# Kernel optimization log

Measured on AMD Instinct MI355X. Metric: run time of the kernel, lower is better.

Reference implementation:

```python
import jax, jax.numpy as jnp
from jax import lax
import numpy as np

DG = 2          # deformable groups
KH = KW = 3     # kernel size
KK = KH * KW
PAD = 1


def setup_inputs() -> dict:
    key = jax.random.key(0)
    k1, k2, k3 = jax.random.split(key, 3)
    B, C, H, W = 4, 64, 128, 128
    O = 64
    x = jax.random.normal(k1, (B, C, H, W), jnp.float32)
    # original inits offset weights to 0 (degenerate: plain conv); use small random
    # weights instead so the irregular bilinear-gather path is actually exercised.
    w_off = jax.random.normal(k2, (DG * 2 * KK, C, KH, KW), jnp.float32) * 0.05
    w_def = jax.random.normal(k3, (O, C, KH, KW), jnp.float32) * (1.0 / np.sqrt(C * KK))
    return {"x": x, "w_off": w_off, "w_def": w_def}


def _deform_conv(x, w_off, w_def):
    B, C, H, W = x.shape
    O = w_def.shape[0]
    Cg = C // DG

    # offset = offset_conv(x): stride 1, pad 1, no bias -> [B, DG*2*KK, H, W]
    offset = lax.conv_general_dilated(
        x, w_off, window_strides=(1, 1), padding=((PAD, PAD), (PAD, PAD)),
        dimension_numbers=("NCHW", "OIHW", "NCHW"))
    # DCN layout: per group, per kernel tap k, channel 2k = dy, 2k+1 = dx
    off = offset.reshape(B, DG, KK, 2, H, W)

    ki, kj = jnp.meshgrid(jnp.arange(KH), jnp.arange(KW), indexing="ij")
    ki = (ki.reshape(KK) - PAD).astype(x.dtype)   # kernel row offsets -1..1
    kj = (kj.reshape(KK) - PAD).astype(x.dtype)
    hh = jnp.arange(H, dtype=x.dtype)
    ww = jnp.arange(W, dtype=x.dtype)

    # sampling positions [B, DG, KK, H, W]
    py = off[:, :, :, 0] + ki[None, None, :, None, None] + hh[None, None, None, :, None]
    px = off[:, :, :, 1] + kj[None, None, :, None, None] + ww[None, None, None, None, :]

    y0 = jnp.floor(py).astype(jnp.int32)
    x0 = jnp.floor(px).astype(jnp.int32)
    dy = py - y0.astype(x.dtype)
    dx = px - x0.astype(x.dtype)

    x_g = x.reshape(B, DG, Cg, H * W)

    def gather(yi, xi):
        # zero padding outside the image
        valid = ((yi >= 0) & (yi < H) & (xi >= 0) & (xi < W)).astype(x.dtype)
        yc = jnp.clip(yi, 0, H - 1)
        xc = jnp.clip(xi, 0, W - 1)
        idx = (yc * W + xc).reshape(B, DG, 1, KK * H * W)
        v = jnp.take_along_axis(x_g, idx, axis=3).reshape(B, DG, Cg, KK, H, W)
        return v * valid[:, :, None]  # broadcast over channel axis

    # bilinear interpolation at learned offset positions
    val = (gather(y0, x0) * ((1 - dy) * (1 - dx))[:, :, None]
           + gather(y0, x0 + 1) * ((1 - dy) * dx)[:, :, None]
           + gather(y0 + 1, x0) * (dy * (1 - dx))[:, :, None]
           + gather(y0 + 1, x0 + 1) * (dy * dx)[:, :, None])

    # weighted accumulation: conv groups = 1, channel dim = DG*Cg
    w = w_def.reshape(O, DG, Cg, KK)
    return jnp.einsum("bgckhw,ogck->bohw", val, w)


def reference(x, w_off, w_def):
    return _deform_conv(x, w_off, w_def)
```

## Files before the change

### kernel.cpp

```cpp
#include <hip/hip_runtime.h>
#include <hip/hip_bf16.h>

typedef _Float16 f16x8 __attribute__((ext_vector_type(8)));
typedef _Float16 f16x2 __attribute__((ext_vector_type(2)));
typedef float f32x4  __attribute__((ext_vector_type(4)));

#define Bn 4
#define Cn 64
#define Hn 128
#define Wn 128
#define HWn 16384

#define XT_BYTES    (Bn*HWn*Cn*2)
#define PKDEF_BYTES (18*4*64*8*2)

static __device__ __forceinline__ unsigned pk_f16(float lo, float hi) {
  union { _Float16 h[2]; unsigned u; } cv;
  cv.h[0] = (_Float16)lo; cv.h[1] = (_Float16)hi;
  return cv.u;
}

__global__ __launch_bounds__(256) void transpose_cast(const float* __restrict__ x,
                                                      ushort* __restrict__ xt) {
  __shared__ float tile[64][65];
  const int t = threadIdx.x;
  const int blk = blockIdx.x;
  const int b = blk >> 8;
  const int pix0 = (blk & 255) * 64;
  const int y = pix0 >> 7, x0 = pix0 & 127;
  const float* xb = x + (b * Cn) * HWn + pix0;
#pragma unroll
  for (int q = 0; q < 16; ++q) {
    int idx = q * 256 + t;
    int c = idx >> 6, p = idx & 63;
    tile[c][p] = xb[c * HWn + p];
  }
  __syncthreads();
  const int p = t & 63, cg = t >> 6;
#pragma unroll
  for (int half = 0; half < 2; ++half) {
    const int seg = cg * 2 + half;
    unsigned u[4];
#pragma unroll
    for (int j = 0; j < 4; ++j)
      u[j] = pk_f16(tile[seg * 8 + 2 * j][p], tile[seg * 8 + 2 * j + 1][p]);
    uint4 v = {u[0], u[1], u[2], u[3]};
    *(uint4*)(xt + (((((b << 7) + y) << 3) + seg) * 128 + x0 + p) * 8) = v;
  }
}

__global__ __launch_bounds__(256) void prep_pack(const float* __restrict__ w_off,
                                                 const float* __restrict__ w_def,
                                                 ushort* __restrict__ pk_def,
                                                 ushort* __restrict__ pk_off) {
  const int t = blockIdx.x * 256 + threadIdx.x;
  if (t < 4608) {
    int lane = t & 63, oc = (t >> 6) & 3, s = t >> 8;
    int g = s / 9, k = s % 9;
    int o = oc * 16 + (lane & 15);
    int cb = g * 32 + (lane >> 4) * 8;
    unsigned u[4];
#pragma unroll
    for (int j = 0; j < 4; ++j)
      u[j] = pk_f16(w_def[(o * Cn + cb + 2 * j) * 9 + k],
                    w_def[(o * Cn + cb + 2 * j + 1) * 9 + k]);
    uint4 v = {u[0], u[1], u[2], u[3]};
    *(uint4*)(pk_def + t * 8) = v;
  } else if (t < 8064) {
    int t2 = t - 4608;
    int lane = t2 & 63, r = t2 >> 6;
    int oc = r % 3, s = r / 3;
    int k = s >> 1, chalf = s & 1;
    int o = oc * 16 + (lane & 15);
    int cb = chalf * 32 + (lane >> 4) * 8;
    unsigned u[4];
#pragma unroll
    for (int j = 0; j < 4; ++j) {
      float lo = (o < 36) ? w_off[(o * Cn + cb + 2 * j) * 9 + k] : 0.f;
      float hi = (o < 36) ? w_off[(o * Cn + cb + 2 * j + 1) * 9 + k] : 0.f;
      u[j] = pk_f16(lo, hi);
    }
    uint4 v = {u[0], u[1], u[2], u[3]};
    *(uint4*)(pk_off + (r * 64 + lane) * 8) = v;
  }
}

__global__ __launch_bounds__(512, 6) void deform_fused(const ushort* __restrict__ xt,
                                                       const ushort* __restrict__ pk_def,
                                                       const ushort* __restrict__ pk_off,
                                                       float* __restrict__ out) {
  __shared__ ushort tile[13 * 23 * 72];
  __shared__ float off_lds[4][36][17];
  const int lane = threadIdx.x & 63;
  const int wid = threadIdx.x >> 6;
  const int pg = wid >> 1, gsel = wid & 1;
  int bid = blockIdx.x;
  bid = (bid & 7) * 128 + (bid >> 3);
  const int b  = bid >> 8;
  const int ty = (bid >> 3) & 31;
  const int tx = bid & 7;
  const int y0t = ty * 4, x0t = tx * 16;
  const int TLY = max(0, y0t - 4), THY = min(127, y0t + 8);
  const int TLX = max(0, x0t - 3), THX = min(127, x0t + 19);
  const int Hd = THY - TLY + 1, Wd = THX - TLX + 1;

  {
    const int xq = threadIdx.x & 31;
    const int r0 = threadIdx.x >> 5;
    const int nr = Hd * 8;
    for (int rr = r0; rr < nr; rr += 16) {
      const int yq = rr >> 3, seg = rr & 7;
      if (xq < Wd) {
        const ushort* src = xt + ((((b << 7) + TLY + yq) << 3) + seg) * 1024 + (TLX + xq) * 8;
        *(uint4*)&tile[(yq * 23 + xq) * 72 + seg * 8] = *(const uint4*)src;
      }
    }
  }
  __syncthreads();

  const int h = y0t + pg;
  const int p = lane & 15, kq = lane >> 4;
  const int w_ = x0t + p;
  const int pixin = (h << 7) + x0t;
  const int su = gsel * 4 + kq;
  const int colb = lane & 15;

  {
    f32x4 oa0 = {0,0,0,0}, oa1 = {0,0,0,0}, oa2 = {0,0,0,0};
    const f16x8* pBo = (const f16x8*)pk_off;
#pragma unroll
    for (int s = 0; s < 18; ++s) {
      const int k = s >> 1, chalf = s & 1;
      int y = h + k / 3 - 1, xx = w_ + k % 3 - 1;
      bool valid = ((unsigned)y < 128u) && ((unsigned)xx < 128u);
      int yc = min(max(y, 0), 127), xc = min(max(xx, 0), 127);
      const int seg = chalf * 4 + kq;
      uint4 t_ = *(const uint4*)&tile[((yc - TLY) * 23 + (xc - TLX)) * 72 + seg * 8];
      if (!valid) { t_.x = 0; t_.y = 0; t_.z = 0; t_.w = 0; }
      union { uint4 u; f16x8 v; } A; A.u = t_;
      if (gsel == 0) {
        oa0 = __builtin_amdgcn_mfma_f32_16x16x32_f16(A.v, pBo[(s*3 + 0)*64 + lane], oa0, 0,0,0);
      } else {
        oa1 = __builtin_amdgcn_mfma_f32_16x16x32_f16(A.v, pBo[(s*3 + 1)*64 + lane], oa1, 0,0,0);
        oa2 = __builtin_amdgcn_mfma_f32_16x16x32_f16(A.v, pBo[(s*3 + 2)*64 + lane], oa2, 0,0,0);
      }
    }
    if (gsel == 0) {
#pragma unroll
      for (int r = 0; r < 4; ++r) off_lds[pg][colb][kq * 4 + r] = oa0[r];
    } else {
#pragma unroll
      for (int r = 0; r < 4; ++r) {
        off_lds[pg][16 + colb][kq * 4 + r] = oa1[r];
        if (colb < 4) off_lds[pg][32 + colb][kq * 4 + r] = oa2[r];
      }
    }
  }
  __syncthreads();

  float offv[18];
#pragma unroll
  for (int j = 0; j < 18; ++j) offv[j] = off_lds[pg][gsel * 18 + j][p];

  f32x4 acc0={0,0,0,0}, acc1={0,0,0,0}, acc2={0,0,0,0}, acc3={0,0,0,0};
  const f16x8* pB = (const f16x8*)pk_def;

#pragma unroll
  for (int j = 0; j < 9; ++j) {
    const int k = j;
    float py = offv[2*j]   + (float)(h  + k / 3 - 1);
    float px = offv[2*j+1] + (float)(w_ + k % 3 - 1);
    float fy = floorf(py), fx = floorf(px);
    int y0 = (int)fy, x0 = (int)fx;
    float dy = py - fy, dx = px - fx;

    bool vy0 = (y0 >= 0) && (y0 < Hn);
    bool vy1 = (y0 >= -1) && (y0 < Hn - 1);
    bool vx0 = (x0 >= 0) && (x0 < Wn);
    bool vx1 = (x0 >= -1) && (x0 < Wn - 1);
    float omdy = 1.f - dy, omdx = 1.f - dx;
    float w00 = (vy0 && vx0) ? omdy * omdx : 0.f;
    float w01 = (vy0 && vx1) ? omdy * dx   : 0.f;
    float w10 = (vy1 && vx0) ? dy * omdx   : 0.f;
    float w11 = (vy1 && vx1) ? dy * dx     : 0.f;

    int iy0 = min(max(y0, 0), Hn - 1), iy1 = min(max(y0 + 1, 0), Hn - 1);
    int ix0 = min(max(x0, 0), Wn - 1), ix1 = min(max(x0 + 1, 0), Wn - 1);

    uint4 c00, c01, c10, c11;
    bool intile = (iy0 >= TLY) && (iy1 <= THY) && (ix0 >= TLX) && (ix1 <= THX);
    if (__all((int)intile)) {
      const int ly0 = iy0 - TLY, ly1 = iy1 - TLY;
      const int lx0 = ix0 - TLX, lx1 = ix1 - TLX;
      c00 = *(const uint4*)&tile[(ly0 * 23 + lx0) * 72 + su * 8];
      c01 = *(const uint4*)&tile[(ly0 * 23 + lx1) * 72 + su * 8];
      c10 = *(const uint4*)&tile[(ly1 * 23 + lx0) * 72 + su * 8];
      c11 = *(const uint4*)&tile[(ly1 * 23 + lx1) * 72 + su * 8];
    } else {
      const int r0g = ((((b << 7) + iy0) << 3) + su) * 128;
      const int r1g = ((((b << 7) + iy1) << 3) + su) * 128;
      c00 = *(const uint4*)(xt + (r0g + ix0) * 8);
      c01 = *(const uint4*)(xt + (r0g + ix1) * 8);
      c10 = *(const uint4*)(xt + (r1g + ix0) * 8);
      c11 = *(const uint4*)(xt + (r1g + ix1) * 8);
    }

    const _Float16 h00 = (_Float16)w00, h01 = (_Float16)w01;
    const _Float16 h10 = (_Float16)w10, h11 = (_Float16)w11;
    const f16x2 W00 = {h00, h00}, W01 = {h01, h01};
    const f16x2 W10 = {h10, h10}, W11 = {h11, h11};
    union U32H { unsigned u; f16x2 h; };
    union { uint4 u; f16x8 v; } A;
#define BILC(comp, fld)                                                        \
    { U32H a0, a1, a2, a3, r;                                                  \
      a0.u = c00.comp; a1.u = c01.comp; a2.u = c10.comp; a3.u = c11.comp;      \
      r.h = a0.h * W00 + a1.h * W01 + a2.h * W10 + a3.h * W11;                 \
      A.u.fld = r.u; }
    BILC(x, x) BILC(y, y) BILC(z, z) BILC(w, w)
#undef BILC

    const int s = gsel * 9 + j;
    acc0 = __builtin_amdgcn_mfma_f32_16x16x32_f16(A.v, pB[(s*4 + 0)*64 + lane], acc0, 0,0,0);
    acc1 = __builtin_amdgcn_mfma_f32_16x16x32_f16(A.v, pB[(s*4 + 1)*64 + lane], acc1, 0,0,0);
    acc2 = __builtin_amdgcn_mfma_f32_16x16x32_f16(A.v, pB[(s*4 + 2)*64 + lane], acc2, 0,0,0);
    acc3 = __builtin_amdgcn_mfma_f32_16x16x32_f16(A.v, pB[(s*4 + 3)*64 + lane], acc3, 0,0,0);
  }

  __syncthreads();
  float* red = (float*)tile;
  if (gsel == 1) {
    *(f32x4*)&red[((pg * 4 + 0) * 64 + lane) * 4] = acc0;
    *(f32x4*)&red[((pg * 4 + 1) * 64 + lane) * 4] = acc1;
    *(f32x4*)&red[((pg * 4 + 2) * 64 + lane) * 4] = acc2;
    *(f32x4*)&red[((pg * 4 + 3) * 64 + lane) * 4] = acc3;
  }
  __syncthreads();
  if (gsel == 0) {
    acc0 += *(const f32x4*)&red[((pg * 4 + 0) * 64 + lane) * 4];
    acc1 += *(const f32x4*)&red[((pg * 4 + 1) * 64 + lane) * 4];
    acc2 += *(const f32x4*)&red[((pg * 4 + 2) * 64 + lane) * 4];
    acc3 += *(const f32x4*)&red[((pg * 4 + 3) * 64 + lane) * 4];
    float* ob = out + pixin + kq * 4;
#pragma unroll
    for (int r = 0; r < 4; ++r) {
      ob[((b*64 +      colb) << 14) + r] = acc0[r];
      ob[((b*64 + 16 + colb) << 14) + r] = acc1[r];
      ob[((b*64 + 32 + colb) << 14) + r] = acc2[r];
      ob[((b*64 + 48 + colb) << 14) + r] = acc3[r];
    }
  }
}

extern "C" void kernel_launch(void* const* d_in, const int* in_sizes, int n_in,
                              void* d_out, int out_size, void* d_ws, size_t ws_size,
                              hipStream_t stream) {
  const float* x     = (const float*)d_in[0];
  const float* w_off = (const float*)d_in[1];
  const float* w_def = (const float*)d_in[2];
  float* out = (float*)d_out;

  char* ws = (char*)d_ws;
  ushort* xt     = (ushort*)ws;
  ushort* pk_def = (ushort*)(ws + XT_BYTES);
  ushort* pk_off = (ushort*)(ws + XT_BYTES + PKDEF_BYTES);

  transpose_cast<<<1024, 256, 0, stream>>>(x, xt);
  prep_pack<<<32, 256, 0, stream>>>(w_off, w_def, pk_def, pk_off);
  deform_fused<<<1024, 512, 0, stream>>>(xt, pk_def, pk_off, out);
}
```

Baseline: 53.70 us.

## Enlarge deform tile to 8 rows, re-layout LDS by channel segment, fp16 offsets

Doubles the output tile height per block (8x16 pixels, 1024 threads, 512 blocks), so the halo-loaded input tile is reused across more rows and the redundant halo loads per output shrink. The LDS tile layout changes from pixel-major with 72-element padding to segment-major planes with a 24-wide row stride, which changes bank access patterns for the gathers. Per-tap pixel offsets and validity for the offset conv are precomputed, and the offset values are stored in LDS as fp16 to save shared memory. Risks: fewer, larger blocks lower the number of resident blocks and raise register pressure, and fp16 offsets lose precision in the bilinear sampling positions.

```diff
diff --git a/kernel.cpp b/kernel.cpp
--- a/kernel.cpp
+++ b/kernel.cpp
@@ -85,34 +85,36 @@
   }
 }
 
-__global__ __launch_bounds__(512, 6) void deform_fused(const ushort* __restrict__ xt,
-                                                       const ushort* __restrict__ pk_def,
-                                                       const ushort* __restrict__ pk_off,
-                                                       float* __restrict__ out) {
-  __shared__ ushort tile[13 * 23 * 72];
-  __shared__ float off_lds[4][36][17];
-  const int lane = threadIdx.x & 63;
-  const int wid = threadIdx.x >> 6;
+#define T_STRIDE (17*24*8)
+__global__ __launch_bounds__(1024, 8) void deform_fused(const ushort* __restrict__ xt,
+                                                        const ushort* __restrict__ pk_def,
+                                                        const ushort* __restrict__ pk_off,
+                                                        float* __restrict__ out) {
+  __shared__ ushort tile[8 * 17 * 24 * 8];
+  __shared__ _Float16 off_lds[8][36][18];
+  const int t = threadIdx.x;
+  const int lane = t & 63;
+  const int wid = t >> 6;
   const int pg = wid >> 1, gsel = wid & 1;
   int bid = blockIdx.x;
-  bid = (bid & 7) * 128 + (bid >> 3);
-  const int b  = bid >> 8;
-  const int ty = (bid >> 3) & 31;
+  bid = (bid & 7) * 64 + (bid >> 3);
+  const int b  = bid >> 7;
+  const int ty = (bid >> 3) & 15;
   const int tx = bid & 7;
-  const int y0t = ty * 4, x0t = tx * 16;
-  const int TLY = max(0, y0t - 4), THY = min(127, y0t + 8);
+  const int y0t = ty * 8, x0t = tx * 16;
+  const int TLY = max(0, y0t - 4), THY = min(127, y0t + 12);
   const int TLX = max(0, x0t - 3), THX = min(127, x0t + 19);
   const int Hd = THY - TLY + 1, Wd = THX - TLX + 1;
 
   {
-    const int xq = threadIdx.x & 31;
-    const int r0 = threadIdx.x >> 5;
+    const int xq = t & 31;
+    const int r0 = t >> 5;
     const int nr = Hd * 8;
-    for (int rr = r0; rr < nr; rr += 16) {
+    for (int rr = r0; rr < nr; rr += 32) {
       const int yq = rr >> 3, seg = rr & 7;
       if (xq < Wd) {
         const ushort* src = xt + ((((b << 7) + TLY + yq) << 3) + seg) * 1024 + (TLX + xq) * 8;
-        *(uint4*)&tile[(yq * 23 + xq) * 72 + seg * 8] = *(const uint4*)src;
+        *(uint4*)&tile[seg * T_STRIDE + (yq * 24 + xq) * 8] = *(const uint4*)src;
       }
     }
   }
@@ -125,18 +127,23 @@
   const int su = gsel * 4 + kq;
   const int colb = lane & 15;
 
+  int pixoff[9]; bool tvalid[9];
+#pragma unroll
+  for (int kk = 0; kk < 9; ++kk) {
+    int yk = h + kk / 3 - 1, xk = w_ + kk % 3 - 1;
+    tvalid[kk] = ((unsigned)yk < 128u) && ((unsigned)xk < 128u);
+    int yc = min(max(yk, 0), 127), xc = min(max(xk, 0), 127);
+    pixoff[kk] = ((yc - TLY) * 24 + (xc - TLX)) * 8;
+  }
+
   {
     f32x4 oa0 = {0,0,0,0}, oa1 = {0,0,0,0}, oa2 = {0,0,0,0};
     const f16x8* pBo = (const f16x8*)pk_off;
 #pragma unroll
     for (int s = 0; s < 18; ++s) {
       const int k = s >> 1, chalf = s & 1;
-      int y = h + k / 3 - 1, xx = w_ + k % 3 - 1;
-      bool valid = ((unsigned)y < 128u) && ((unsigned)xx < 128u);
-      int yc = min(max(y, 0), 127), xc = min(max(xx, 0), 127);
-      const int seg = chalf * 4 + kq;
-      uint4 t_ = *(const uint4*)&tile[((yc - TLY) * 23 + (xc - TLX)) * 72 + seg * 8];
-      if (!valid) { t_.x = 0; t_.y = 0; t_.z = 0; t_.w = 0; }
+      uint4 t_ = *(const uint4*)&tile[(chalf * 4 + kq) * T_STRIDE + pixoff[k]];
+      if (!tvalid[k]) { t_.x = 0; t_.y = 0; t_.z = 0; t_.w = 0; }
       union { uint4 u; f16x8 v; } A; A.u = t_;
       if (gsel == 0) {
         oa0 = __builtin_amdgcn_mfma_f32_16x16x32_f16(A.v, pBo[(s*3 + 0)*64 + lane], oa0, 0,0,0);
@@ -147,12 +154,12 @@
     }
     if (gsel == 0) {
 #pragma unroll
-      for (int r = 0; r < 4; ++r) off_lds[pg][colb][kq * 4 + r] = oa0[r];
+      for (int r = 0; r < 4; ++r) off_lds[pg][colb][kq * 4 + r] = (_Float16)oa0[r];
     } else {
 #pragma unroll
       for (int r = 0; r < 4; ++r) {
-        off_lds[pg][16 + colb][kq * 4 + r] = oa1[r];
-        if (colb < 4) off_lds[pg][32 + colb][kq * 4 + r] = oa2[r];
+        off_lds[pg][16 + colb][kq * 4 + r] = (_Float16)oa1[r];
+        if (colb < 4) off_lds[pg][32 + colb][kq * 4 + r] = (_Float16)oa2[r];
       }
     }
   }
@@ -160,7 +167,7 @@
 
   float offv[18];
 #pragma unroll
-  for (int j = 0; j < 18; ++j) offv[j] = off_lds[pg][gsel * 18 + j][p];
+  for (int j = 0; j < 18; ++j) offv[j] = (float)off_lds[pg][gsel * 18 + j][p];
 
   f32x4 acc0={0,0,0,0}, acc1={0,0,0,0}, acc2={0,0,0,0}, acc3={0,0,0,0};
   const f16x8* pB = (const f16x8*)pk_def;
@@ -190,12 +197,13 @@
     uint4 c00, c01, c10, c11;
     bool intile = (iy0 >= TLY) && (iy1 <= THY) && (ix0 >= TLX) && (ix1 <= THX);
     if (__all((int)intile)) {
+      const int base = su * T_STRIDE;
       const int ly0 = iy0 - TLY, ly1 = iy1 - TLY;
       const int lx0 = ix0 - TLX, lx1 = ix1 - TLX;
-      c00 = *(const uint4*)&tile[(ly0 * 23 + lx0) * 72 + su * 8];
-      c01 = *(const uint4*)&tile[(ly0 * 23 + lx1) * 72 + su * 8];
-      c10 = *(const uint4*)&tile[(ly1 * 23 + lx0) * 72 + su * 8];
-      c11 = *(const uint4*)&tile[(ly1 * 23 + lx1) * 72 + su * 8];
+      c00 = *(const uint4*)&tile[base + (ly0 * 24 + lx0) * 8];
+      c01 = *(const uint4*)&tile[base + (ly0 * 24 + lx1) * 8];
+      c10 = *(const uint4*)&tile[base + (ly1 * 24 + lx0) * 8];
+      c11 = *(const uint4*)&tile[base + (ly1 * 24 + lx1) * 8];
     } else {
       const int r0g = ((((b << 7) + iy0) << 3) + su) * 128;
       const int r1g = ((((b << 7) + iy1) << 3) + su) * 128;
@@ -266,5 +274,5 @@
 
   transpose_cast<<<1024, 256, 0, stream>>>(x, xt);
   prep_pack<<<32, 256, 0, stream>>>(w_off, w_def, pk_def, pk_off);
-  deform_fused<<<1024, 512, 0, stream>>>(xt, pk_def, pk_off, out);
-}
+  deform_fused<<<512, 1024, 0, stream>>>(xt, pk_def, pk_off, out);
+}
```

Result: faster. 49.94 us (-7.0%).
